# Optimization experiments

Hardware: AMD Instinct MI355X
Metric: run time of the kernel (lower is better)

The kernel has to match this reference:

```python
import jax, jax.numpy as jnp
import numpy as np

NUM_CLASSES = 128
NUM_DOMAINS = 6
FEAT_DIM = 256
B = 524288
MOMENTUM = 0.9
MARGIN = 1.0


def setup_inputs() -> dict:
    key = jax.random.key(0)
    k1, k2, k3, k4, k5, k6 = jax.random.split(key, 6)
    mu_tilde = jax.random.normal(k1, (B, FEAT_DIM), dtype=jnp.float32)
    anchors = jax.random.normal(k2, (NUM_DOMAINS, NUM_CLASSES, FEAT_DIM), dtype=jnp.float32)
    domain_means = jax.random.normal(k3, (NUM_DOMAINS, FEAT_DIM), dtype=jnp.float32)
    domain_vars = jax.random.uniform(k4, (NUM_DOMAINS, FEAT_DIM), dtype=jnp.float32)
    y_true = jax.random.randint(k5, (B,), 0, NUM_CLASSES, dtype=jnp.int32)
    d_true = jax.random.randint(k6, (B,), 0, NUM_DOMAINS, dtype=jnp.int32)
    return {"mu_tilde": mu_tilde, "anchors": anchors, "domain_means": domain_means,
            "domain_vars": domain_vars, "y_true": y_true, "d_true": d_true}


def reference(mu_tilde, anchors, domain_means, domain_vars, y_true, d_true):
    m = MOMENTUM
    one = jnp.asarray(1.0, mu_tilde.dtype)

    # ---- update(): fused per-(domain,class) segment mean + EMA anchor write ----
    seg = d_true.astype(jnp.int32) * NUM_CLASSES + y_true.astype(jnp.int32)
    n_seg = NUM_DOMAINS * NUM_CLASSES
    seg_sum = jax.ops.segment_sum(mu_tilde, seg, num_segments=n_seg)          # (Nd*C, D)
    seg_cnt = jax.ops.segment_sum(jnp.ones((B,), mu_tilde.dtype), seg, num_segments=n_seg)
    seg_mean = seg_sum / jnp.maximum(seg_cnt, one)[:, None]
    has_samples = (seg_cnt > 0).reshape(NUM_DOMAINS, NUM_CLASSES, 1)
    batch_anchor = seg_mean.reshape(NUM_DOMAINS, NUM_CLASSES, FEAT_DIM)
    new_anchors = jnp.where(has_samples, m * anchors + (1.0 - m) * batch_anchor, anchors)

    # ---- update(): per-domain mean/var (unbiased) + EMA ----
    d_sum = jax.ops.segment_sum(mu_tilde, d_true, num_segments=NUM_DOMAINS)
    d_sq = jax.ops.segment_sum(mu_tilde * mu_tilde, d_true, num_segments=NUM_DOMAINS)
    d_cnt = jax.ops.segment_sum(jnp.ones((B,), mu_tilde.dtype), d_true, num_segments=NUM_DOMAINS)
    safe_cnt = jnp.maximum(d_cnt, one)[:, None]
    b_mean = d_sum / safe_cnt
    b_var = (d_sq - safe_cnt * b_mean * b_mean) / jnp.maximum(d_cnt - 1.0, one)[:, None]
    g = (d_cnt > 1)[:, None]
    new_means = jnp.where(g, m * domain_means + (1.0 - m) * b_mean, domain_means)
    new_vars = jnp.where(g, m * domain_vars + (1.0 - m) * b_var, domain_vars)

    # ---- caa_loss() on updated anchors (all anchors initialized) ----
    class_mean = new_anchors.mean(axis=0, keepdims=True)                      # (1, C, D)
    loss_intra = jnp.mean((new_anchors - class_mean) ** 2)                    # avg of per-class MSE
    A_mean = new_anchors.mean(axis=0)                                         # (C, D)
    sq = jnp.sum(A_mean * A_mean, axis=1)
    d2 = sq[:, None] + sq[None, :] - 2.0 * (A_mean @ A_mean.T)
    off_diag = ~jnp.eye(NUM_CLASSES, dtype=bool)
    d2_safe = jnp.where(off_diag, jnp.maximum(d2, 1e-12), 1.0)
    dist = jnp.sqrt(d2_safe)
    loss_inter = jnp.sum(jnp.where(off_diag, jax.nn.relu(MARGIN - dist), 0.0))
    loss_inter = loss_inter / (NUM_CLASSES * (NUM_CLASSES - 1))
    loss_caa = loss_intra + loss_inter

    # ---- stats_align_loss() on updated stats ----
    global_mean = new_means.mean(axis=0)
    global_var = new_vars.mean(axis=0)
    loss_mean = jnp.mean((new_means - global_mean) ** 2)   # sum_d mse / Nd
    loss_var = jnp.mean((new_vars - global_var) ** 2)
    mu_mean = mu_tilde.mean(axis=0)
    mu_var = jnp.mean(mu_tilde * mu_tilde, axis=0) - mu_mean * mu_mean        # biased var
    loss_mu_mean = jnp.mean((mu_mean - global_mean) ** 2)
    loss_mu_var = jnp.mean((mu_var - global_var) ** 2)
    loss_stats = loss_mean + loss_var + loss_mu_mean + loss_mu_var

    return new_anchors, new_means, new_vars, loss_caa + loss_stats
```

## Files before the change

### kernel.cpp

```cpp
#include <hip/hip_runtime.h>

#define B_N   524288
#define FEAT  256
#define NC    128
#define ND    6
#define NSEG  768
#define CAP   1024

#define ZERO_WORDS 3852

typedef float f4v __attribute__((ext_vector_type(4)));

__device__ __forceinline__ float block_reduce(float v, float* lds) {
  #pragma unroll
  for (int o = 32; o > 0; o >>= 1) v += __shfl_down(v, o, 64);
  int wid = threadIdx.x >> 6, lane = threadIdx.x & 63;
  if (lane == 0) lds[wid] = v;
  __syncthreads();
  int nw = (blockDim.x + 63) >> 6;
  v = 0.0f;
  if (wid == 0 && lane < nw) v = lds[lane];
  if (wid == 0) {
    #pragma unroll
    for (int o = 4; o > 0; o >>= 1) v += __shfl_down(v, o, 64);
  }
  return v;
}

#define SCHUNK 4096
#define SCAT_BLOCKS (B_N / SCHUNK)
__global__ __launch_bounds__(1024)
void scatter_k(const int* __restrict__ y, const int* __restrict__ dmn,
               int* __restrict__ cursor, int* __restrict__ slots) {
  __shared__ int lcnt[NSEG];
  __shared__ int lbase[NSEG];
  int t = threadIdx.x;
  if (t < NSEG) lcnt[t] = 0;
  __syncthreads();
  int base = blockIdx.x * SCHUNK;
  int segr[4], lposr[4];
  #pragma unroll
  for (int k = 0; k < 4; ++k) {
    int i = base + t + k * 1024;
    int seg = dmn[i] * NC + y[i];
    segr[k] = seg;
    lposr[k] = atomicAdd(&lcnt[seg], 1);
  }
  __syncthreads();
  if (t < NSEG) lbase[t] = atomicAdd(&cursor[t], lcnt[t]);
  __syncthreads();
  #pragma unroll
  for (int k = 0; k < 4; ++k) {
    int i = base + t + k * 1024;
    int p = lbase[segr[k]] + lposr[k];
    if (p < CAP) slots[segr[k] * CAP + p] = i;
  }
}

__global__ __launch_bounds__(512, 6)
void segreduce_k(const float* __restrict__ mu, const int* __restrict__ slots,
                 const int* __restrict__ cursor, float* __restrict__ seg_sum,
                 float* __restrict__ d_sum_acc, float* __restrict__ d_sq_acc,
                 float* __restrict__ d_cnt) {
  int seg = blockIdx.x;
  int cnt = cursor[seg];
  if (cnt > CAP) cnt = CAP;
  int dom = seg >> 7;
  int t  = threadIdx.x;
  int rr = t >> 6;
  int dq = t & 63;
  const int* sl = slots + seg * CAP;
  const size_t doff = (size_t)(dq << 2);

  float ax=0,ay=0,az=0,aw=0, aqx=0,aqy=0,aqz=0,aqw=0;
  float bx=0,by=0,bz=0,bw=0, bqx=0,bqy=0,bqz=0,bqw=0;

  int r = rr;
  int row0 = (r     < cnt) ? sl[r]     : 0;
  int row1 = (r + 8 < cnt) ? sl[r + 8] : 0;
  while (r + 8 < cnt) {
    int n0 = (r + 16 < cnt) ? sl[r + 16] : 0;
    int n1 = (r + 24 < cnt) ? sl[r + 24] : 0;
    const f4v v0 = __builtin_nontemporal_load(
        reinterpret_cast<const f4v*>(mu + (size_t)row0 * FEAT + doff));
    const f4v v1 = __builtin_nontemporal_load(
        reinterpret_cast<const f4v*>(mu + (size_t)row1 * FEAT + doff));
    ax += v0.x; ay += v0.y; az += v0.z; aw += v0.w;
    aqx += v0.x*v0.x; aqy += v0.y*v0.y; aqz += v0.z*v0.z; aqw += v0.w*v0.w;
    bx += v1.x; by += v1.y; bz += v1.z; bw += v1.w;
    bqx += v1.x*v1.x; bqy += v1.y*v1.y; bqz += v1.z*v1.z; bqw += v1.w*v1.w;
    r += 16; row0 = n0; row1 = n1;
  }
  if (r < cnt) {
    const f4v v0 = __builtin_nontemporal_load(
        reinterpret_cast<const f4v*>(mu + (size_t)row0 * FEAT + doff));
    ax += v0.x; ay += v0.y; az += v0.z; aw += v0.w;
    aqx += v0.x*v0.x; aqy += v0.y*v0.y; aqz += v0.z*v0.z; aqw += v0.w*v0.w;
  }
  ax += bx; ay += by; az += bz; aw += bw;
  aqx += bqx; aqy += bqy; aqz += bqz; aqw += bqw;

  __shared__ float4 redS[512];
  __shared__ float4 redQ[512];
  redS[t] = make_float4(ax, ay, az, aw);
  redQ[t] = make_float4(aqx, aqy, aqz, aqw);
  __syncthreads();
  if (rr == 0) {
    float4 s = redS[t], q = redQ[t];
    #pragma unroll
    for (int g = 1; g < 8; ++g) {
      float4 a = redS[t + 64*g]; s.x+=a.x; s.y+=a.y; s.z+=a.z; s.w+=a.w;
      float4 b = redQ[t + 64*g]; q.x+=b.x; q.y+=b.y; q.z+=b.z; q.w+=b.w;
    }
    *reinterpret_cast<float4*>(seg_sum + (size_t)seg * FEAT + (dq << 2)) = s;
    int base = dom * FEAT + (dq << 2);
    atomicAdd(&d_sum_acc[base+0], s.x); atomicAdd(&d_sum_acc[base+1], s.y);
    atomicAdd(&d_sum_acc[base+2], s.z); atomicAdd(&d_sum_acc[base+3], s.w);
    atomicAdd(&d_sq_acc[base+0], q.x);  atomicAdd(&d_sq_acc[base+1], q.y);
    atomicAdd(&d_sq_acc[base+2], q.z);  atomicAdd(&d_sq_acc[base+3], q.w);
  }
  if (t == 0) atomicAdd(&d_cnt[dom], (float)cnt);
}

__global__ void anchors_k(const float* __restrict__ anchors, const float* __restrict__ seg_sum,
                          const int* __restrict__ cursor, float* __restrict__ out_anchors,
                          float* __restrict__ class_mean, float* __restrict__ sqv,
                          float* __restrict__ loss_acc) {
  int c = blockIdx.x;
  int d = threadIdx.x;
  float na[ND];
  float cm = 0.0f;
  #pragma unroll
  for (int dom = 0; dom < ND; ++dom) {
    int segi = dom * NC + c;
    int cnt = cursor[segi];
    float s = seg_sum[(size_t)segi * FEAT + d];
    float mean = s / fmaxf((float)cnt, 1.0f);
    float a = anchors[(size_t)segi * FEAT + d];
    float v = (cnt > 0) ? (0.9f * a + 0.1f * mean) : a;
    out_anchors[(size_t)segi * FEAT + d] = v;
    na[dom] = v;
    cm += v;
  }
  cm /= 6.0f;
  class_mean[c * FEAT + d] = cm;
  float li = 0.0f;
  #pragma unroll
  for (int dom = 0; dom < ND; ++dom) { float e = na[dom] - cm; li += e * e; }

  __shared__ float rbuf[8];
  float r1 = block_reduce(li, rbuf);
  __syncthreads();
  float r2 = block_reduce(cm * cm, rbuf);
  if (threadIdx.x == 0) { atomicAdd(&loss_acc[0], r1); sqv[c] = r2; }
}

__global__ __launch_bounds__(256)
void tail_k(const float* __restrict__ class_mean, const float* __restrict__ sqv,
            const float* __restrict__ dmeans, const float* __restrict__ dvars,
            const float* __restrict__ d_sum_acc, const float* __restrict__ d_sq_acc,
            const float* __restrict__ d_cnt, float* __restrict__ out_means,
            float* __restrict__ out_vars, float* __restrict__ loss_acc,
            int* __restrict__ done_ctr, float* __restrict__ out_loss) {
  int b = blockIdx.x;
  int t = threadIdx.x;
  __shared__ float rbuf[8];

  if (b < NC) {
    __shared__ float Ai[FEAT];
    __shared__ float dots[256];
    Ai[t] = class_mean[b * FEAT + t];
    __syncthreads();
    int j = t & 127, h = t >> 7;
    const float* Aj  = class_mean + (size_t)j * FEAT + h * 128;
    const float* Aih = Ai + h * 128;
    float dot = 0.0f;
    #pragma unroll 8
    for (int k = 0; k < 128; ++k) dot += Aih[k] * Aj[k];
    dots[t] = dot;
    __syncthreads();
    float contrib = 0.0f;
    if (h == 0 && j != b) {
      float d2 = sqv[b] + sqv[j] - 2.0f * (dots[j] + dots[j + 128]);
      d2 = fmaxf(d2, 1e-12f);
      contrib = fmaxf(1.0f - sqrtf(d2), 0.0f);
    }
    float r = block_reduce(contrib, rbuf);
    if (t == 0) atomicAdd(&loss_acc[1], r);
  } else {
    int d = t;
    float nm[ND], nv[ND];
    float gm = 0.0f, gv = 0.0f, tsum = 0.0f, tsq = 0.0f;
    #pragma unroll
    for (int dom = 0; dom < ND; ++dom) {
      float cf = d_cnt[dom];
      float safe = fmaxf(cf, 1.0f);
      float su = d_sum_acc[dom * FEAT + d];
      float sq = d_sq_acc[dom * FEAT + d];
      tsum += su; tsq += sq;
      float bm = su / safe;
      float bv = (sq - safe * bm * bm) / fmaxf(cf - 1.0f, 1.0f);
      float m0 = dmeans[dom * FEAT + d], v0 = dvars[dom * FEAT + d];
      bool g = cf > 1.0f;
      float m1 = g ? (0.9f * m0 + 0.1f * bm) : m0;
      float v1 = g ? (0.9f * v0 + 0.1f * bv) : v0;
      out_means[dom * FEAT + d] = m1;
      out_vars[dom * FEAT + d]  = v1;
      nm[dom] = m1; nv[dom] = v1; gm += m1; gv += v1;
    }
    gm /= 6.0f; gv /= 6.0f;
    float lm = 0.0f, lv = 0.0f;
    #pragma unroll
    for (int dom = 0; dom < ND; ++dom) {
      float e = nm[dom] - gm; lm += e * e;
      float f = nv[dom] - gv; lv += f * f;
    }
    float mum = tsum * (1.0f / (float)B_N);
    float muv = tsq * (1.0f / (float)B_N) - mum * mum;
    float lmm = (mum - gm) * (mum - gm);
    float lmv = (muv - gv) * (muv - gv);
    float val = (lm + lv) * (1.0f / 1536.0f) + (lmm + lmv) * (1.0f / 256.0f);
    float r = block_reduce(val, rbuf);
    if (t == 0) atomicAdd(&loss_acc[2], r);
  }

  if (t == 0) {
    __threadfence();
    int old = atomicAdd(done_ctr, 1);
    if (old == NC) {
      float li = atomicAdd(&loss_acc[0], 0.0f);
      float le = atomicAdd(&loss_acc[1], 0.0f);
      float ls = atomicAdd(&loss_acc[2], 0.0f);
      *out_loss = li * (1.0f / 196608.0f)
                + le * (1.0f / 16256.0f)
                + ls;
    }
  }
}

extern "C" void kernel_launch(void* const* d_in, const int* in_sizes, int n_in,
                              void* d_out, int out_size, void* d_ws, size_t ws_size,
                              hipStream_t stream) {
  const float* mu      = (const float*)d_in[0];
  const float* anchors = (const float*)d_in[1];
  const float* dmeans  = (const float*)d_in[2];
  const float* dvars   = (const float*)d_in[3];
  const int*   y       = (const int*)d_in[4];
  const int*   dmn     = (const int*)d_in[5];

  float* out = (float*)d_out;
  float* out_anchors = out;
  float* out_means   = out + 196608;
  float* out_vars    = out + 198144;
  float* out_loss    = out + 199680;

  float* wsf       = (float*)d_ws;
  int*   cursor    = (int*)d_ws;
  float* d_cnt     = wsf + 768;
  float* d_sum_acc = wsf + 776;
  float* d_sq_acc  = wsf + 2312;
  float* loss_acc  = wsf + 3848;
  int*   done_ctr  = (int*)d_ws + 3851;
  float* seg_sum   = wsf + ZERO_WORDS;
  float* class_mean= seg_sum + NSEG * FEAT;
  float* sqv       = class_mean + NC * FEAT;
  int*   slots     = (int*)(sqv + 128);

  hipMemsetAsync(d_ws, 0, ZERO_WORDS * sizeof(float), stream);
  scatter_k  <<<SCAT_BLOCKS, 1024, 0, stream>>>(y, dmn, cursor, slots);
  segreduce_k<<<NSEG, 512, 0, stream>>>(mu, slots, cursor, seg_sum, d_sum_acc, d_sq_acc, d_cnt);
  anchors_k  <<<NC, 256, 0, stream>>>(anchors, seg_sum, cursor, out_anchors, class_mean, sqv, loss_acc);
  tail_k     <<<NC + 1, 256, 0, stream>>>(class_mean, sqv, dmeans, dvars, d_sum_acc, d_sq_acc,
                                          d_cnt, out_means, out_vars, loss_acc, done_ctr, out_loss);
}
```

Before: 132.1 us.

## Fuse anchor EMA into segment reduce and use contiguous per-wave row ranges

The anchor EMA update now happens inside segreduce_k, which writes out_anchors directly. This removes the seg_sum intermediate buffer and its write and read round trip. The old anchors kernel becomes a lighter class-mean kernel that reads the updated anchors. Each wave in segreduce now handles a contiguous chunk of slot indices instead of a stride-8 interleave, which changes the slot-read locality and the summation order. The main memory traffic is still the gathered mu reads, so the expected saving is small.

```diff
diff --git a/kernel.cpp b/kernel.cpp
--- a/kernel.cpp
+++ b/kernel.cpp
@@ -59,7 +59,8 @@
 
 __global__ __launch_bounds__(512, 6)
 void segreduce_k(const float* __restrict__ mu, const int* __restrict__ slots,
-                 const int* __restrict__ cursor, float* __restrict__ seg_sum,
+                 const int* __restrict__ cursor, const float* __restrict__ anchors,
+                 float* __restrict__ out_anchors,
                  float* __restrict__ d_sum_acc, float* __restrict__ d_sq_acc,
                  float* __restrict__ d_cnt) {
   int seg = blockIdx.x;
@@ -72,15 +73,18 @@
   const int* sl = slots + seg * CAP;
   const size_t doff = (size_t)(dq << 2);
 
+  int c0 = (cnt * rr) >> 3;
+  int c1 = (cnt * (rr + 1)) >> 3;
+
   float ax=0,ay=0,az=0,aw=0, aqx=0,aqy=0,aqz=0,aqw=0;
   float bx=0,by=0,bz=0,bw=0, bqx=0,bqy=0,bqz=0,bqw=0;
 
-  int r = rr;
-  int row0 = (r     < cnt) ? sl[r]     : 0;
-  int row1 = (r + 8 < cnt) ? sl[r + 8] : 0;
-  while (r + 8 < cnt) {
-    int n0 = (r + 16 < cnt) ? sl[r + 16] : 0;
-    int n1 = (r + 24 < cnt) ? sl[r + 24] : 0;
+  int r = c0;
+  int row0 = (r     < c1) ? sl[r]     : 0;
+  int row1 = (r + 1 < c1) ? sl[r + 1] : 0;
+  while (r + 1 < c1) {
+    int n0 = (r + 2 < c1) ? sl[r + 2] : 0;
+    int n1 = (r + 3 < c1) ? sl[r + 3] : 0;
     const f4v v0 = __builtin_nontemporal_load(
         reinterpret_cast<const f4v*>(mu + (size_t)row0 * FEAT + doff));
     const f4v v1 = __builtin_nontemporal_load(
@@ -89,9 +93,9 @@
     aqx += v0.x*v0.x; aqy += v0.y*v0.y; aqz += v0.z*v0.z; aqw += v0.w*v0.w;
     bx += v1.x; by += v1.y; bz += v1.z; bw += v1.w;
     bqx += v1.x*v1.x; bqy += v1.y*v1.y; bqz += v1.z*v1.z; bqw += v1.w*v1.w;
-    r += 16; row0 = n0; row1 = n1;
-  }
-  if (r < cnt) {
+    r += 2; row0 = n0; row1 = n1;
+  }
+  if (r < c1) {
     const f4v v0 = __builtin_nontemporal_load(
         reinterpret_cast<const f4v*>(mu + (size_t)row0 * FEAT + doff));
     ax += v0.x; ay += v0.y; az += v0.z; aw += v0.w;
@@ -104,6 +108,8 @@
   __shared__ float4 redQ[512];
   redS[t] = make_float4(ax, ay, az, aw);
   redQ[t] = make_float4(aqx, aqy, aqz, aqw);
+  float4 aold;
+  if (rr == 0) aold = *reinterpret_cast<const float4*>(anchors + (size_t)seg * FEAT + doff);
   __syncthreads();
   if (rr == 0) {
     float4 s = redS[t], q = redQ[t];
@@ -112,7 +118,14 @@
       float4 a = redS[t + 64*g]; s.x+=a.x; s.y+=a.y; s.z+=a.z; s.w+=a.w;
       float4 b = redQ[t + 64*g]; q.x+=b.x; q.y+=b.y; q.z+=b.z; q.w+=b.w;
     }
-    *reinterpret_cast<float4*>(seg_sum + (size_t)seg * FEAT + (dq << 2)) = s;
+    float inv01 = 0.1f / fmaxf((float)cnt, 1.0f);
+    float4 o;
+    if (cnt > 0) {
+      o.x = 0.9f*aold.x + s.x*inv01; o.y = 0.9f*aold.y + s.y*inv01;
+      o.z = 0.9f*aold.z + s.z*inv01; o.w = 0.9f*aold.w + s.w*inv01;
+    } else o = aold;
+    *reinterpret_cast<float4*>(out_anchors + (size_t)seg * FEAT + doff) = o;
+
     int base = dom * FEAT + (dq << 2);
     atomicAdd(&d_sum_acc[base+0], s.x); atomicAdd(&d_sum_acc[base+1], s.y);
     atomicAdd(&d_sum_acc[base+2], s.z); atomicAdd(&d_sum_acc[base+3], s.w);
@@ -122,23 +135,16 @@
   if (t == 0) atomicAdd(&d_cnt[dom], (float)cnt);
 }
 
-__global__ void anchors_k(const float* __restrict__ anchors, const float* __restrict__ seg_sum,
-                          const int* __restrict__ cursor, float* __restrict__ out_anchors,
-                          float* __restrict__ class_mean, float* __restrict__ sqv,
-                          float* __restrict__ loss_acc) {
+__global__ void classmean_k(const float* __restrict__ out_anchors,
+                            float* __restrict__ class_mean, float* __restrict__ sqv,
+                            float* __restrict__ loss_acc) {
   int c = blockIdx.x;
   int d = threadIdx.x;
   float na[ND];
   float cm = 0.0f;
   #pragma unroll
   for (int dom = 0; dom < ND; ++dom) {
-    int segi = dom * NC + c;
-    int cnt = cursor[segi];
-    float s = seg_sum[(size_t)segi * FEAT + d];
-    float mean = s / fmaxf((float)cnt, 1.0f);
-    float a = anchors[(size_t)segi * FEAT + d];
-    float v = (cnt > 0) ? (0.9f * a + 0.1f * mean) : a;
-    out_anchors[(size_t)segi * FEAT + d] = v;
+    float v = out_anchors[(size_t)(dom * NC + c) * FEAT + d];
     na[dom] = v;
     cm += v;
   }
@@ -261,15 +267,15 @@
   float* d_sq_acc  = wsf + 2312;
   float* loss_acc  = wsf + 3848;
   int*   done_ctr  = (int*)d_ws + 3851;
-  float* seg_sum   = wsf + ZERO_WORDS;
-  float* class_mean= seg_sum + NSEG * FEAT;
+  float* class_mean= wsf + ZERO_WORDS;
   float* sqv       = class_mean + NC * FEAT;
   int*   slots     = (int*)(sqv + 128);
 
   hipMemsetAsync(d_ws, 0, ZERO_WORDS * sizeof(float), stream);
   scatter_k  <<<SCAT_BLOCKS, 1024, 0, stream>>>(y, dmn, cursor, slots);
-  segreduce_k<<<NSEG, 512, 0, stream>>>(mu, slots, cursor, seg_sum, d_sum_acc, d_sq_acc, d_cnt);
-  anchors_k  <<<NC, 256, 0, stream>>>(anchors, seg_sum, cursor, out_anchors, class_mean, sqv, loss_acc);
+  segreduce_k<<<NSEG, 512, 0, stream>>>(mu, slots, cursor, anchors, out_anchors,
+                                        d_sum_acc, d_sq_acc, d_cnt);
+  classmean_k<<<NC, 256, 0, stream>>>(out_anchors, class_mean, sqv, loss_acc);
   tail_k     <<<NC + 1, 256, 0, stream>>>(class_mean, sqv, dmeans, dvars, d_sum_acc, d_sq_acc,
                                           d_cnt, out_means, out_vars, loss_acc, done_ctr, out_loss);
 }
```

After: 131.2 us. No clear change (-0.7%).
